# Kernel tuning notes

Hardware: AMD Instinct MI355X
Metric: run time of the kernel (lower is better)

Reference implementation:

```python
import jax, jax.numpy as jnp
import numpy as np

B = 64        # number of tasks (sequential steps)
D = 512       # knowledge_representation_dim == understanding_representation_dim
M = 8192      # memory_slots
GAMMA = 0.95  # memory_gamma


def setup_inputs() -> dict:
    key = jax.random.key(0)
    k1, k2, k3, k4 = jax.random.split(key, 4)
    ortho = jax.nn.initializers.orthogonal()
    return {
        "k": jax.random.normal(k1, (B, 1, D), jnp.float32),
        "u": jax.random.normal(k2, (B, 1, D), jnp.float32),
        "memory_knowledge": ortho(k3, (D, M), jnp.float32),
        "memory_understanding": ortho(k4, (D, M), jnp.float32),
        "beta_param": jnp.float32(0.0),
        "memory_gamma": jnp.float32(GAMMA),
    }


def reference(k, u, memory_knowledge, memory_understanding, beta_param, memory_gamma):
    n_slots = memory_knowledge.shape[1]
    slot_ids = jnp.arange(n_slots)
    beta = jax.nn.sigmoid(beta_param)

    def step(carry, xs):
        MK, MU, w_w, w_u, w_lu = carry
        k_task, u_task = xs  # each [1, D]
        # cosine similarity of the task key against every memory column: [1, M]
        sim = (k_task @ MK) / (
            jnp.linalg.norm(k_task, axis=-1, keepdims=True)
            * jnp.linalg.norm(MK, axis=0, keepdims=True)
        )
        w_r = jax.nn.softmax(sim, axis=-1)[0]  # [M]
        # zero out the least-used slot (argmin of usage weights)
        keep = (slot_ids != jnp.argmin(w_u))[None, :]  # [1, M]
        MK = jnp.where(keep, MK, 0.0)
        MU = jnp.where(keep, MU, 0.0)
        # usage / write / least-used weight updates
        w_u = memory_gamma * w_u + w_r + w_w
        w_w = beta * jnp.mean(w_r) + (1.0 - beta) * w_lu  # [M] via broadcast of scalar mean
        w_lu = (slot_ids == jnp.argmin(w_u)).astype(MK.dtype)  # one-hot least-used
        # rank-1 write of understanding, then read refined understanding, then write knowledge
        MU = MU + u_task[0][:, None] * w_w[None, :]  # [D, M]
        u_ref = w_r @ MK.T  # [D] -- read uses MK after zeroing, before its write
        MK = MK + k_task[0][:, None] * w_w[None, :]  # [D, M]
        return (MK, MU, w_w, w_u, w_lu), u_ref

    zeros = jnp.zeros((n_slots,), memory_knowledge.dtype)
    init = (memory_knowledge, memory_understanding, zeros, zeros, zeros)
    _, u_refined = jax.lax.scan(step, init, (k, u))
    return u_refined[:, None, :]  # [B, 1, D]
```

## Files before the change

### kernel.cpp

```cpp
#include <hip/hip_runtime.h>
#include <math.h>

#define BB 64
#define DD 512
#define MM 8192
#define K2T 512
#define K2C 16

typedef unsigned long long u64;

template<int CTRL>
__device__ __forceinline__ float dpp_addf(float x) {
    int y = __builtin_amdgcn_update_dpp(0, __float_as_int(x), CTRL, 0xF, 0xF, true);
    return x + __int_as_float(y);
}
__device__ __forceinline__ float wave_sum64(float x) {
    x = dpp_addf<0x111>(x); x = dpp_addf<0x112>(x); x = dpp_addf<0x114>(x); x = dpp_addf<0x118>(x);
    x = dpp_addf<0x142>(x); x = dpp_addf<0x143>(x);
    return __int_as_float(__builtin_amdgcn_readlane(__float_as_int(x), 63));
}
template<int CTRL>
__device__ __forceinline__ u64 dpp_min_step(u64 k) {
    unsigned lo = (unsigned)k, hi = (unsigned)(k >> 32);
    unsigned nlo = (unsigned)__builtin_amdgcn_update_dpp((int)0xFFFFFFFFu, (int)lo, CTRL, 0xF, 0xF, false);
    unsigned nhi = (unsigned)__builtin_amdgcn_update_dpp((int)0xFFFFFFFFu, (int)hi, CTRL, 0xF, 0xF, false);
    u64 nk = (((u64)nhi) << 32) | (u64)nlo;
    return nk < k ? nk : k;
}
__device__ __forceinline__ u64 wave_min64_lane63(u64 k) {
    k = dpp_min_step<0x111>(k); k = dpp_min_step<0x112>(k); k = dpp_min_step<0x114>(k);
    k = dpp_min_step<0x118>(k); k = dpp_min_step<0x142>(k); k = dpp_min_step<0x143>(k);
    return k;
}
__device__ __forceinline__ u64 wave_min8(u64 k) {
    k = dpp_min_step<0x111>(k); k = dpp_min_step<0x112>(k); k = dpp_min_step<0x114>(k);
    unsigned lo = (unsigned)__builtin_amdgcn_readlane((int)(unsigned)k, 7);
    unsigned hi = (unsigned)__builtin_amdgcn_readlane((int)(unsigned)(k >> 32), 7);
    return (((u64)hi) << 32) | (u64)lo;
}
__device__ __forceinline__ float readlane_f(float v, int l) {
    return __int_as_float(__builtin_amdgcn_readlane(__float_as_int(v), l));
}

struct K0Smem {
    float Ks[BB][129];
    float Gs[BB][BB];
};
struct K1Smem {
    float Ks[64 * 65];
    float Ms[64 * 65];
    float sq[4 * 64];
};
#define KA_SMEM ((sizeof(K0Smem) > sizeof(K1Smem)) ? sizeof(K0Smem) : sizeof(K1Smem))

__global__ __launch_bounds__(256) void ka_gram_s0(const float* __restrict__ K, const float* __restrict__ MK0,
                                                  float* __restrict__ G, float* __restrict__ Pfx,
                                                  float* __restrict__ S0p, float* __restrict__ n2p) {
    __shared__ __align__(16) char blob[KA_SMEM];
    const int tid = threadIdx.x;

    if (blockIdx.x == 0) {
        K0Smem* sm = (K0Smem*)blob;
        const int ti = ((tid >> 4) & 15) << 2;
        const int tj = (tid & 15) << 2;
        float acc[4][4];
        #pragma unroll
        for (int i = 0; i < 4; ++i)
            #pragma unroll
            for (int j = 0; j < 4; ++j) acc[i][j] = 0.f;
        for (int d0 = 0; d0 < DD; d0 += 128) {
            #pragma unroll
            for (int i = 0; i < 32; ++i) {
                int e = i * 256 + tid; int r = e >> 7, c = e & 127;
                sm->Ks[r][c] = K[r * DD + d0 + c];
            }
            __syncthreads();
            for (int dl = 0; dl < 128; ++dl) {
                float rv[4], cv[4];
                #pragma unroll
                for (int i = 0; i < 4; ++i) rv[i] = sm->Ks[ti + i][dl];
                #pragma unroll
                for (int j = 0; j < 4; ++j) cv[j] = sm->Ks[tj + j][dl];
                #pragma unroll
                for (int i = 0; i < 4; ++i)
                    #pragma unroll
                    for (int j = 0; j < 4; ++j) acc[i][j] += rv[i] * cv[j];
            }
            __syncthreads();
        }
        #pragma unroll
        for (int i = 0; i < 4; ++i)
            #pragma unroll
            for (int j = 0; j < 4; ++j) {
                G[(ti + i) * BB + tj + j] = acc[i][j];
                sm->Gs[ti + i][tj + j] = acc[i][j];
            }
        __syncthreads();
        const int s = tid & 63, w = tid >> 6;
        for (int rr = 0; rr < 16; ++rr) {
            int row = w * 16 + rr;
            float x = (s < row) ? sm->Gs[row][s] : 0.f;
            #pragma unroll
            for (int o = 1; o < 64; o <<= 1) {
                float y = __shfl_down(x, o);
                if (s + o < 64) x += y;
            }
            Pfx[row * BB + s] = x;
        }
        return;
    }

    K1Smem* sm = (K1Smem*)blob;
    const int b = blockIdx.x - 1;
    const int lane = tid & 63, w = tid >> 6;
    const int jb = (b & 127) * 64;
    const int by = b >> 7;
    const int dbase = by * 256;
    const int t4 = ((w << 2) | (lane >> 4)) << 2;
    const int jq0 = lane & 15;
    float acc[4][4];
    #pragma unroll
    for (int i = 0; i < 4; ++i)
        #pragma unroll
        for (int q = 0; q < 4; ++q) acc[i][q] = 0.f;
    float sqa = 0.f;
    for (int dt = 0; dt < 4; ++dt) {
        int d0 = dbase + dt * 64;
        #pragma unroll
        for (int i = 0; i < 16; ++i) {
            int e = i * 256 + tid; int r = e >> 6, c = e & 63;
            sm->Ks[r * 65 + c] = K[r * DD + d0 + c];
            float m = MK0[(d0 + r) * MM + jb + c];
            sm->Ms[r * 65 + c] = m;
            sqa += m * m;
        }
        __syncthreads();
        #pragma unroll 4
        for (int dl = 0; dl < 64; ++dl) {
            float kv[4], mv[4];
            #pragma unroll
            for (int i = 0; i < 4; ++i) kv[i] = sm->Ks[(t4 + i) * 65 + dl];
            #pragma unroll
            for (int q = 0; q < 4; ++q) mv[q] = sm->Ms[dl * 65 + jq0 + 16 * q];
            #pragma unroll
            for (int i = 0; i < 4; ++i)
                #pragma unroll
                for (int q = 0; q < 4; ++q) acc[i][q] += kv[i] * mv[q];
        }
        __syncthreads();
    }
    #pragma unroll
    for (int i = 0; i < 4; ++i)
        #pragma unroll
        for (int q = 0; q < 4; ++q)
            S0p[by * BB * MM + (t4 + i) * MM + jb + jq0 + 16 * q] = acc[i][q];
    sm->sq[w * 64 + lane] = sqa;
    __syncthreads();
    if (w == 0) n2p[by * MM + jb + lane] =
        sm->sq[lane] + sm->sq[64 + lane] + sm->sq[128 + lane] + sm->sq[192 + lane];
}

__global__ __launch_bounds__(256) void k1b_ecold(const float* __restrict__ S0p,
                                                 const float* __restrict__ G,
                                                 const float* __restrict__ Pfx,
                                                 const float* __restrict__ n2p,
                                                 const float* __restrict__ bp,
                                                 float* __restrict__ Ecold) {
    __shared__ float Pfx0s[BB], invks[BB], k2s[BB];
    int tid = threadIdx.x;
    int j = blockIdx.x * 256 + tid;
    if (tid < BB) {
        float g = G[tid * BB + tid];
        k2s[tid] = g;
        invks[tid] = __builtin_amdgcn_rsqf(g);
        Pfx0s[tid] = Pfx[tid * BB + 0];
    }
    const float beta = 1.f / (1.f + expf(-bp[0]));
    const float cuni = beta / (float)MM;
    float n2c = n2p[j] + n2p[MM + j];
    __syncthreads();
    for (int t = 0; t < BB; ++t) {
        float s0 = S0p[t * MM + j] + S0p[(BB + t) * MM + j];
        float d_ = s0 + cuni * Pfx0s[t];
        float cosv = d_ * invks[t] * __builtin_amdgcn_rsqf(n2c);
        float ee = __expf(cosv);
        Ecold[t * MM + j] = ee;
        n2c = n2c + 2.f * cuni * d_ + cuni * cuni * k2s[t];
    }
}

__global__ __launch_bounds__(256) void ks_rowsum(const float* __restrict__ Ecold, float* __restrict__ Scold) {
    __shared__ float sw[4];
    int t = blockIdx.x, tid = threadIdx.x;
    int lane = tid & 63, wid = tid >> 6;
    float s = 0.f;
    #pragma unroll
    for (int i = 0; i < 32; ++i) s += Ecold[t * MM + i * 256 + tid];
    #pragma unroll
    for (int o = 32; o > 0; o >>= 1) s += __shfl_down(s, o);
    if (lane == 0) sw[wid] = s;
    __syncthreads();
    if (tid == 0) Scold[t] = sw[0] + sw[1] + sw[2] + sw[3];
}

struct ScanSmem {
    u64   red[2][8];
    float EtabL[BB * BB];
    float EcTabL[BB * BB];
    float invSL[BB];
    float SL[BB];
    int   endL[BB];
    float invS_bc;
};
struct K3Smem {
    float Ws[64 * 65];
    float Msub[64 * 65];
};
#define SMEM_BYTES ((sizeof(ScanSmem) > sizeof(K3Smem)) ? sizeof(ScanSmem) : sizeof(K3Smem))

__global__ __launch_bounds__(512) void k23_scan_u1(const float* __restrict__ Ecold,
                                                   const float* __restrict__ G,
                                                   const float* __restrict__ Pfx,
                                                   const float* __restrict__ Scoldg,
                                                   const float* __restrict__ bp,
                                                   const float* __restrict__ gp,
                                                   const float* __restrict__ MK0,
                                                   float* __restrict__ Etab_g,
                                                   float* __restrict__ EcTab_g,
                                                   float* __restrict__ Sg,
                                                   float* __restrict__ invSg,
                                                   int*   __restrict__ endTab_g,
                                                   int*   __restrict__ hcolg,
                                                   float* __restrict__ parts) {
    __shared__ __align__(16) char smem_raw[SMEM_BYTES];
    const int tid = threadIdx.x;

    if (blockIdx.x != 0) {
        K3Smem* sm = (K3Smem*)smem_raw;
        const int tile = blockIdx.x - 1;
        const int d0 = (tile & 7) * 64;
        const int by = tile >> 3;
        const bool act = tid < 256;
        const int lane = tid & 63, w = tid >> 6;
        const int t4 = ((w << 2) | (lane >> 4)) << 2;
        const int dq0 = lane & 15;
        float acc[4][4];
        #pragma unroll
        for (int i = 0; i < 4; ++i)
            #pragma unroll
            for (int q = 0; q < 4; ++q) acc[i][q] = 0.f;
        for (int sub = 0; sub < 4; ++sub) {
            int jb = by * 256 + sub * 64;
            if (act) {
                #pragma unroll
                for (int i = 0; i < 16; ++i) {
                    int e = i * 256 + tid; int r = e >> 6, c = e & 63;
                    sm->Ws[r * 65 + c] = Ecold[r * MM + jb + c];
                    sm->Msub[r * 65 + c] = MK0[(d0 + r) * MM + jb + c];
                }
            }
            __syncthreads();
            if (act) {
                #pragma unroll 4
                for (int jl = 0; jl < 64; ++jl) {
                    float wv[4], mv[4];
                    #pragma unroll
                    for (int i = 0; i < 4; ++i) wv[i] = sm->Ws[(t4 + i) * 65 + jl];
                    #pragma unroll
                    for (int q = 0; q < 4; ++q) mv[q] = sm->Msub[(dq0 + 16 * q) * 65 + jl];
                    #pragma unroll
                    for (int i = 0; i < 4; ++i)
                        #pragma unroll
                        for (int q = 0; q < 4; ++q) acc[i][q] += wv[i] * mv[q];
                }
            }
            __syncthreads();
        }
        if (act) {
            #pragma unroll
            for (int i = 0; i < 4; ++i)
                #pragma unroll
                for (int q = 0; q < 4; ++q)
                    parts[(by * 64 + t4 + i) * DD + d0 + dq0 + 16 * q] = acc[i][q];
        }
        return;
    }

    ScanSmem* sm = (ScanSmem*)smem_raw;
    const int lane = tid & 63;
    const int wid = tid >> 6;
    const bool w0 = (wid == 0);

    const float beta  = 1.f / (1.f + expf(-bp[0]));
    const float gamma = gp[0];
    const float cuni  = beta / (float)MM;
    const float omb   = 1.f - beta;

    if (tid < BB) sm->endL[tid] = BB;

    const float4* Ec4 = reinterpret_cast<const float4*>(Ecold);

    float wu[K2C], eb0[K2C], eb1[K2C];
    #pragma unroll
    for (int c = 0; c < K2C; ++c) wu[c] = 0.f;
    #pragma unroll
    for (int i = 0; i < K2C / 4; ++i) {
        float4 v = Ec4[i * K2T + tid];
        eb0[4 * i + 0] = v.x; eb0[4 * i + 1] = v.y; eb0[4 * i + 2] = v.z; eb0[4 * i + 3] = v.w;
    }

    float slot_n2 = 0.f, slot_E = 0.f, slot_ec = 0.f, slot_ecpf = 0.f, wu_hot = 0.f;
    int   slot_j = -1;
    bool  slot_act = false;

    float grow_c = 0.f, pfx_c = 0.f, Ssc_c = 0.f;
    if (w0) { grow_c = G[lane]; pfx_c = Pfx[lane]; Ssc_c = Scoldg[0]; }
    __syncthreads();

    auto step = [&](int t, float (&cur)[K2C], float (&nxt)[K2C]) {
        int j0; float minval;
        if (t == 0) { j0 = 0; minval = 0.f; }
        else {
            u64 pm = sm->red[t & 1][lane & 7];
            pm = wave_min8(pm);
            j0 = (int)(pm & 0xFFFFFFFFu);
            minval = __uint_as_float((unsigned)(pm >> 32));
        }
        const float cuni_t = (t == 0) ? 0.f : cuni;

        float latev = 0.f;
        if (w0 && lane == t) latev = Ecold[t * MM + j0];
        if (w0 && t + 1 < BB) {
            int js = (lane == t) ? j0 : slot_j;
            if (slot_act || lane == t) slot_ecpf = Ecold[(t + 1) * MM + js];
        }
        float grow_n = 0.f, pfx_n = 0.f, Ssc_n = 0.f;
        if (w0 && t + 1 < BB) {
            grow_n = G[(t + 1) * BB + lane];
            pfx_n  = Pfx[(t + 1) * BB + lane];
            Ssc_n  = Scoldg[t + 1];
        }
        __builtin_amdgcn_sched_barrier(0);
        if (t + 1 < BB) {
            #pragma unroll
            for (int i = 0; i < K2C / 4; ++i) {
                float4 v = Ec4[(t + 1) * (MM / 4) + i * K2T + tid];
                nxt[4 * i + 0] = v.x; nxt[4 * i + 1] = v.y; nxt[4 * i + 2] = v.z; nxt[4 * i + 3] = v.w;
            }
        }
        __builtin_amdgcn_sched_barrier(0);

        float invS = 0.f, S = 0.f, e_true = 0.f;
        bool fresh = false;
        if (w0) {
            const float k2t  = readlane_f(grow_c, t);
            const float invk = __builtin_amdgcn_rsqf(k2t);

            u64 sup = __ballot(slot_act && (slot_j == j0));
            const bool has_sup = (sup != 0ull);
            const int  ssup = has_sup ? (int)__builtin_ctzll(sup) : 0;

            float myDelta = 0.f;
            if (slot_act) {
                float d_ = cuni * pfx_c;
                if (lane >= 1) d_ += omb * grow_c;
                e_true = __expf(d_ * invk * __builtin_amdgcn_rsqf(slot_n2));
                myDelta = e_true - slot_ec;
                slot_E = e_true;
                slot_n2 = slot_n2 + 2.f * cuni * d_ + cuni * cuni * k2t;
            }

            S = Ssc_c + wave_sum64(myDelta);
            invS = __builtin_amdgcn_rcpf(S);
            sm->invS_bc = invS;

            if (slot_act) {
                float ww = cuni + ((t >= 2 && lane == t - 1) ? omb : 0.f);
                wu_hot = fmaf(gamma, wu_hot, fmaf(e_true, invS, ww));
            }

            float trans_wu = readlane_f(wu_hot, ssup);
            float trans_E  = readlane_f(e_true, ssup);
            if (lane == t) {
                slot_j = j0;
                float ww0 = cuni + ((t >= 1) ? omb : 0.f);
                slot_n2 = ww0 * ww0 * k2t;
                slot_act = true;
                if (has_sup) { wu_hot = trans_wu; slot_E = trans_E; }
                fresh = !has_sup;
            }
            if (has_sup) {
                if (lane == ssup) slot_act = false;
                if (lane == t) sm->endL[ssup] = t;
            }
        }

        asm volatile("s_waitcnt lgkmcnt(0)" ::: "memory");
        __builtin_amdgcn_s_barrier();
        asm volatile("" ::: "memory");
        if (!w0) invS = sm->invS_bc;

        float vmin = 0.f; int jmin = 0;
        #pragma unroll
        for (int i = 0; i < 4; ++i) {
            #pragma unroll
            for (int q = 0; q < 4; ++q) {
                int c = i * 4 + q;
                float wun = fmaf(gamma, wu[c], fmaf(cur[c], invS, cuni_t));
                wu[c] = wun;
                int j = i * 2048 + (tid << 2) + q;
                if (c == 0) { vmin = wun; jmin = j; }
                else if (wun < vmin) { vmin = wun; jmin = j; }
            }
        }
        u64 key = (((u64)__float_as_uint(vmin)) << 32) | (unsigned)jmin;

        if (((j0 >> 2) & (K2T - 1)) == tid) {
            int cj = ((j0 >> 11) << 2) | (j0 & 3);
            #pragma unroll
            for (int c = 0; c < K2C; ++c) if (c == cj) wu[c] = __builtin_inff();
        }

        if (w0) {
            u64 skey = (slot_act && !fresh)
                     ? ((((u64)__float_as_uint(wu_hot)) << 32) | (unsigned)slot_j) : ~0ull;
            key = skey < key ? skey : key;
        }
        key = wave_min64_lane63(key);
        if (lane == 63) sm->red[(t + 1) & 1][wid] = key;

        if (w0) {
            if (lane == t) slot_ec = latev;
            if (fresh) {
                slot_E  = latev;
                wu_hot  = fmaf(gamma, minval, fmaf(latev, invS, cuni_t));
            }
            sm->EtabL[t * BB + lane]  = slot_E;
            sm->EcTabL[t * BB + lane] = slot_ec;
            if (lane == 0) { sm->invSL[t] = invS; sm->SL[t] = S; }
            if (slot_act) slot_ec = slot_ecpf;
            grow_c = grow_n; pfx_c = pfx_n; Ssc_c = Ssc_n;
        }

        asm volatile("s_waitcnt lgkmcnt(0)" ::: "memory");
        __builtin_amdgcn_s_barrier();
        asm volatile("" ::: "memory");
    };

    #pragma unroll 1
    for (int th = 0; th < BB; th += 2) {
        step(th, eb0, eb1);
        step(th + 1, eb1, eb0);
    }

    for (int i = tid; i < BB * BB; i += K2T) {
        Etab_g[i]  = sm->EtabL[i];
        EcTab_g[i] = sm->EcTabL[i];
    }
    if (tid < BB) {
        Sg[tid] = sm->SL[tid];
        invSg[tid] = sm->invSL[tid];
        endTab_g[tid] = sm->endL[tid];
    }
    if (w0) hcolg[lane] = slot_j;
}

__global__ __launch_bounds__(512) void k3b_gather(const float* __restrict__ MK0, const int* __restrict__ hcolg,
                                                  float* __restrict__ MKhot) {
    int i = blockIdx.x, d = threadIdx.x;
    int h = hcolg[i];
    MKhot[i * DD + d] = MK0[d * MM + h];
}

__global__ __launch_bounds__(512) void k4_final(const float* __restrict__ parts,
                                                const float* __restrict__ K,
                                                const float* __restrict__ Etab,
                                                const float* __restrict__ EcTab,
                                                const int*   __restrict__ endTab,
                                                const float* __restrict__ Sg,
                                                const float* __restrict__ invSg,
                                                const float* __restrict__ MKhot,
                                                const float* __restrict__ bp,
                                                float* __restrict__ out) {
    __shared__ float Arow[BB];
    __shared__ float Drow[BB];
    int t = blockIdx.x, d = threadIdx.x;
    if (d < BB) {
        const float beta = 1.f / (1.f + expf(-bp[0]));
        const float cuni = beta / (float)MM;
        const float omb  = 1.f - beta;
        int s = d;
        float Ev = Etab[t * BB + s];
        int endv = endTab[s];
        bool act = (s <= t) && (t < endv);
        float S = Sg[t], invS = invSg[t];
        float ev = act ? Ev : 0.f;
        float x = ev;
        #pragma unroll
        for (int o = 1; o < 64; o <<= 1) {
            float y = __shfl_down(x, o);
            if (s + o < 64) x += y;
        }
        float suf = x - ev;
        float arow = 0.f;
        if (s < t) {
            float Qe = S - suf;
            arow = cuni * Qe;
            if (s >= 1 && act) arow += omb * Ev;
            arow *= invS;
        }
        Arow[s] = arow;
        Drow[s] = act ? (-invS * EcTab[t * BB + s]) : 0.f;
    }
    __syncthreads();
    float isv = invSg[t];
    float s1 = 0.f;
    #pragma unroll
    for (int p = 0; p < 32; ++p) s1 += parts[(p * 64 + t) * DD + d];
    float s2 = 0.f;
    for (int i = 0; i < BB; ++i) s2 += Drow[i] * MKhot[i * DD + d];
    float s3 = 0.f;
    for (int i = 0; i < BB; ++i) s3 += Arow[i] * K[i * DD + d];
    out[t * DD + d] = isv * s1 + s2 + s3;
}

extern "C" void kernel_launch(void* const* d_in, const int* in_sizes, int n_in,
                              void* d_out, int out_size, void* d_ws, size_t ws_size,
                              hipStream_t stream) {
    const float* K   = (const float*)d_in[0];
    const float* MK0 = (const float*)d_in[2];
    const float* bp  = (const float*)d_in[4];
    const float* gp  = (const float*)d_in[5];

    float* ws    = (float*)d_ws;
    float* G     = ws;
    float* Pfx   = G + 4096;
    float* S0p   = Pfx + 4096;
    float* n2p   = S0p + 1048576;
    float* Ecold = n2p + 16384;
    float* Scold = Ecold + 524288;
    float* Etab  = Scold + 64;
    float* EcTab = Etab + 4096;
    float* Sarr  = EcTab + 4096;
    float* invS  = Sarr + 64;
    float* MKhot = invS + 64;
    float* parts = MKhot + 32768;
    int*   hcol  = (int*)(parts + 1048576);
    int*   endT  = hcol + 64;
    float* out   = (float*)d_out;

    ka_gram_s0  <<<257, 256, 0, stream>>>(K, MK0, G, Pfx, S0p, n2p);
    k1b_ecold   <<<32, 256, 0, stream>>>(S0p, G, Pfx, n2p, bp, Ecold);
    ks_rowsum   <<<64, 256, 0, stream>>>(Ecold, Scold);
    k23_scan_u1 <<<257, 512, 0, stream>>>(Ecold, G, Pfx, Scold, bp, gp, MK0,
                                          Etab, EcTab, Sarr, invS, endT, hcol, parts);
    k3b_gather  <<<64, 512, 0, stream>>>(MK0, hcol, MKhot);
    k4_final    <<<64, 512, 0, stream>>>(parts, K, Etab, EcTab, endT, Sarr, invS, MKhot, bp, out);
}
```

Before: 220.8 us.

## Deepen scan prefetch, tree-reduce argmin, widen ecold grid, store tables directly

The scan block now prefetches Ecold rows two steps ahead using a three-buffer rotation, and replaces the sequential per-thread argmin with a pairwise tree over packed 64-bit keys. Per-step tables go straight to global memory instead of being staged in shared memory and copied out at the end. k1b_ecold runs 128 blocks of 64 threads with software-prefetched S0p loads, and the GEMM side of k23 drops to 255 worker blocks that loop over tiles. The aim is to shorten the serial scan's critical path and spread the ecold pass over more CUs, at the cost of extra registers and uneven GEMM tile distribution.

```diff
diff --git a/kernel.cpp b/kernel.cpp
--- a/kernel.cpp
+++ b/kernel.cpp
@@ -160,16 +160,16 @@
         sm->sq[lane] + sm->sq[64 + lane] + sm->sq[128 + lane] + sm->sq[192 + lane];
 }
 
-__global__ __launch_bounds__(256) void k1b_ecold(const float* __restrict__ S0p,
-                                                 const float* __restrict__ G,
-                                                 const float* __restrict__ Pfx,
-                                                 const float* __restrict__ n2p,
-                                                 const float* __restrict__ bp,
-                                                 float* __restrict__ Ecold) {
+__global__ __launch_bounds__(64) void k1b_ecold(const float* __restrict__ S0p,
+                                                const float* __restrict__ G,
+                                                const float* __restrict__ Pfx,
+                                                const float* __restrict__ n2p,
+                                                const float* __restrict__ bp,
+                                                float* __restrict__ Ecold) {
     __shared__ float Pfx0s[BB], invks[BB], k2s[BB];
     int tid = threadIdx.x;
-    int j = blockIdx.x * 256 + tid;
-    if (tid < BB) {
+    int j = blockIdx.x * 64 + tid;
+    {
         float g = G[tid * BB + tid];
         k2s[tid] = g;
         invks[tid] = __builtin_amdgcn_rsqf(g);
@@ -179,13 +179,21 @@
     const float cuni = beta / (float)MM;
     float n2c = n2p[j] + n2p[MM + j];
     __syncthreads();
+    float pa = S0p[j];
+    float pb = S0p[BB * MM + j];
     for (int t = 0; t < BB; ++t) {
-        float s0 = S0p[t * MM + j] + S0p[(BB + t) * MM + j];
+        float na = 0.f, nb = 0.f;
+        if (t + 1 < BB) {
+            na = S0p[(t + 1) * MM + j];
+            nb = S0p[(BB + t + 1) * MM + j];
+        }
+        float s0 = pa + pb;
         float d_ = s0 + cuni * Pfx0s[t];
         float cosv = d_ * invks[t] * __builtin_amdgcn_rsqf(n2c);
         float ee = __expf(cosv);
         Ecold[t * MM + j] = ee;
         n2c = n2c + 2.f * cuni * d_ + cuni * cuni * k2s[t];
+        pa = na; pb = nb;
     }
 }
 
@@ -205,10 +213,6 @@
 
 struct ScanSmem {
     u64   red[2][8];
-    float EtabL[BB * BB];
-    float EcTabL[BB * BB];
-    float invSL[BB];
-    float SL[BB];
     int   endL[BB];
     float invS_bc;
 };
@@ -237,51 +241,53 @@
 
     if (blockIdx.x != 0) {
         K3Smem* sm = (K3Smem*)smem_raw;
-        const int tile = blockIdx.x - 1;
-        const int d0 = (tile & 7) * 64;
-        const int by = tile >> 3;
-        const bool act = tid < 256;
-        const int lane = tid & 63, w = tid >> 6;
-        const int t4 = ((w << 2) | (lane >> 4)) << 2;
-        const int dq0 = lane & 15;
-        float acc[4][4];
-        #pragma unroll
-        for (int i = 0; i < 4; ++i)
-            #pragma unroll
-            for (int q = 0; q < 4; ++q) acc[i][q] = 0.f;
-        for (int sub = 0; sub < 4; ++sub) {
-            int jb = by * 256 + sub * 64;
+        for (int tile = blockIdx.x - 1; tile < 256; tile += 255) {
+            const int d0 = (tile & 7) * 64;
+            const int by = tile >> 3;
+            const bool act = tid < 256;
+            const int lane = tid & 63, w = tid >> 6;
+            const int t4 = ((w << 2) | (lane >> 4)) << 2;
+            const int dq0 = lane & 15;
+            float acc[4][4];
+            #pragma unroll
+            for (int i = 0; i < 4; ++i)
+                #pragma unroll
+                for (int q = 0; q < 4; ++q) acc[i][q] = 0.f;
+            for (int sub = 0; sub < 4; ++sub) {
+                int jb = by * 256 + sub * 64;
+                if (act) {
+                    #pragma unroll
+                    for (int i = 0; i < 16; ++i) {
+                        int e = i * 256 + tid; int r = e >> 6, c = e & 63;
+                        sm->Ws[r * 65 + c] = Ecold[r * MM + jb + c];
+                        sm->Msub[r * 65 + c] = MK0[(d0 + r) * MM + jb + c];
+                    }
+                }
+                __syncthreads();
+                if (act) {
+                    #pragma unroll 4
+                    for (int jl = 0; jl < 64; ++jl) {
+                        float wv[4], mv[4];
+                        #pragma unroll
+                        for (int i = 0; i < 4; ++i) wv[i] = sm->Ws[(t4 + i) * 65 + jl];
+                        #pragma unroll
+                        for (int q = 0; q < 4; ++q) mv[q] = sm->Msub[(dq0 + 16 * q) * 65 + jl];
+                        #pragma unroll
+                        for (int i = 0; i < 4; ++i)
+                            #pragma unroll
+                            for (int q = 0; q < 4; ++q) acc[i][q] += wv[i] * mv[q];
+                    }
+                }
+                __syncthreads();
+            }
             if (act) {
                 #pragma unroll
-                for (int i = 0; i < 16; ++i) {
-                    int e = i * 256 + tid; int r = e >> 6, c = e & 63;
-                    sm->Ws[r * 65 + c] = Ecold[r * MM + jb + c];
-                    sm->Msub[r * 65 + c] = MK0[(d0 + r) * MM + jb + c];
-                }
+                for (int i = 0; i < 4; ++i)
+                    #pragma unroll
+                    for (int q = 0; q < 4; ++q)
+                        parts[(by * 64 + t4 + i) * DD + d0 + dq0 + 16 * q] = acc[i][q];
             }
             __syncthreads();
-            if (act) {
-                #pragma unroll 4
-                for (int jl = 0; jl < 64; ++jl) {
-                    float wv[4], mv[4];
-                    #pragma unroll
-                    for (int i = 0; i < 4; ++i) wv[i] = sm->Ws[(t4 + i) * 65 + jl];
-                    #pragma unroll
-                    for (int q = 0; q < 4; ++q) mv[q] = sm->Msub[(dq0 + 16 * q) * 65 + jl];
-                    #pragma unroll
-                    for (int i = 0; i < 4; ++i)
-                        #pragma unroll
-                        for (int q = 0; q < 4; ++q) acc[i][q] += wv[i] * mv[q];
-                }
-            }
-            __syncthreads();
-        }
-        if (act) {
-            #pragma unroll
-            for (int i = 0; i < 4; ++i)
-                #pragma unroll
-                for (int q = 0; q < 4; ++q)
-                    parts[(by * 64 + t4 + i) * DD + d0 + dq0 + 16 * q] = acc[i][q];
         }
         return;
     }
@@ -300,13 +306,15 @@
 
     const float4* Ec4 = reinterpret_cast<const float4*>(Ecold);
 
-    float wu[K2C], eb0[K2C], eb1[K2C];
+    float wu[K2C], e0[K2C], e1[K2C], e2[K2C];
     #pragma unroll
     for (int c = 0; c < K2C; ++c) wu[c] = 0.f;
     #pragma unroll
     for (int i = 0; i < K2C / 4; ++i) {
         float4 v = Ec4[i * K2T + tid];
-        eb0[4 * i + 0] = v.x; eb0[4 * i + 1] = v.y; eb0[4 * i + 2] = v.z; eb0[4 * i + 3] = v.w;
+        e0[4 * i + 0] = v.x; e0[4 * i + 1] = v.y; e0[4 * i + 2] = v.z; e0[4 * i + 3] = v.w;
+        float4 u = Ec4[(MM / 4) + i * K2T + tid];
+        e1[4 * i + 0] = u.x; e1[4 * i + 1] = u.y; e1[4 * i + 2] = u.z; e1[4 * i + 3] = u.w;
     }
 
     float slot_n2 = 0.f, slot_E = 0.f, slot_ec = 0.f, slot_ecpf = 0.f, wu_hot = 0.f;
@@ -317,7 +325,7 @@
     if (w0) { grow_c = G[lane]; pfx_c = Pfx[lane]; Ssc_c = Scoldg[0]; }
     __syncthreads();
 
-    auto step = [&](int t, float (&cur)[K2C], float (&nxt)[K2C]) {
+    auto step = [&](int t, float (&cur)[K2C], float (&ld)[K2C]) {
         int j0; float minval;
         if (t == 0) { j0 = 0; minval = 0.f; }
         else {
@@ -341,11 +349,11 @@
             Ssc_n  = Scoldg[t + 1];
         }
         __builtin_amdgcn_sched_barrier(0);
-        if (t + 1 < BB) {
+        if (t + 2 < BB) {
             #pragma unroll
             for (int i = 0; i < K2C / 4; ++i) {
-                float4 v = Ec4[(t + 1) * (MM / 4) + i * K2T + tid];
-                nxt[4 * i + 0] = v.x; nxt[4 * i + 1] = v.y; nxt[4 * i + 2] = v.z; nxt[4 * i + 3] = v.w;
+                float4 v = Ec4[(t + 2) * (MM / 4) + i * K2T + tid];
+                ld[4 * i + 0] = v.x; ld[4 * i + 1] = v.y; ld[4 * i + 2] = v.z; ld[4 * i + 3] = v.w;
             }
         }
         __builtin_amdgcn_sched_barrier(0);
@@ -400,7 +408,7 @@
         asm volatile("" ::: "memory");
         if (!w0) invS = sm->invS_bc;
 
-        float vmin = 0.f; int jmin = 0;
+        u64 kk[K2C];
         #pragma unroll
         for (int i = 0; i < 4; ++i) {
             #pragma unroll
@@ -409,11 +417,15 @@
                 float wun = fmaf(gamma, wu[c], fmaf(cur[c], invS, cuni_t));
                 wu[c] = wun;
                 int j = i * 2048 + (tid << 2) + q;
-                if (c == 0) { vmin = wun; jmin = j; }
-                else if (wun < vmin) { vmin = wun; jmin = j; }
-            }
-        }
-        u64 key = (((u64)__float_as_uint(vmin)) << 32) | (unsigned)jmin;
+                kk[c] = (((u64)__float_as_uint(wun)) << 32) | (unsigned)j;
+            }
+        }
+        #pragma unroll
+        for (int s = 8; s >= 1; s >>= 1)
+            #pragma unroll
+            for (int c = 0; c < s; ++c)
+                kk[c] = kk[c + s] < kk[c] ? kk[c + s] : kk[c];
+        u64 key = kk[0];
 
         if (((j0 >> 2) & (K2T - 1)) == tid) {
             int cj = ((j0 >> 11) << 2) | (j0 & 3);
@@ -435,9 +447,9 @@
                 slot_E  = latev;
                 wu_hot  = fmaf(gamma, minval, fmaf(latev, invS, cuni_t));
             }
-            sm->EtabL[t * BB + lane]  = slot_E;
-            sm->EcTabL[t * BB + lane] = slot_ec;
-            if (lane == 0) { sm->invSL[t] = invS; sm->SL[t] = S; }
+            Etab_g[t * BB + lane]  = slot_E;
+            EcTab_g[t * BB + lane] = slot_ec;
+            if (lane == 0) { invSg[t] = invS; Sg[t] = S; }
             if (slot_act) slot_ec = slot_ecpf;
             grow_c = grow_n; pfx_c = pfx_n; Ssc_c = Ssc_n;
         }
@@ -448,20 +460,14 @@
     };
 
     #pragma unroll 1
-    for (int th = 0; th < BB; th += 2) {
-        step(th, eb0, eb1);
-        step(th + 1, eb1, eb0);
-    }
-
-    for (int i = tid; i < BB * BB; i += K2T) {
-        Etab_g[i]  = sm->EtabL[i];
-        EcTab_g[i] = sm->EcTabL[i];
-    }
-    if (tid < BB) {
-        Sg[tid] = sm->SL[tid];
-        invSg[tid] = sm->invSL[tid];
-        endTab_g[tid] = sm->endL[tid];
-    }
+    for (int th = 0; th < 63; th += 3) {
+        step(th + 0, e0, e2);
+        step(th + 1, e1, e0);
+        step(th + 2, e2, e1);
+    }
+    step(63, e0, e2);
+
+    if (tid < BB) endTab_g[tid] = sm->endL[tid];
     if (w0) hcolg[lane] = slot_j;
 }
 
@@ -550,9 +556,9 @@
     float* out   = (float*)d_out;
 
     ka_gram_s0  <<<257, 256, 0, stream>>>(K, MK0, G, Pfx, S0p, n2p);
-    k1b_ecold   <<<32, 256, 0, stream>>>(S0p, G, Pfx, n2p, bp, Ecold);
+    k1b_ecold   <<<128, 64, 0, stream>>>(S0p, G, Pfx, n2p, bp, Ecold);
     ks_rowsum   <<<64, 256, 0, stream>>>(Ecold, Scold);
-    k23_scan_u1 <<<257, 512, 0, stream>>>(Ecold, G, Pfx, Scold, bp, gp, MK0,
+    k23_scan_u1 <<<256, 512, 0, stream>>>(Ecold, G, Pfx, Scold, bp, gp, MK0,
                                           Etab, EcTab, Sarr, invS, endT, hcol, parts);
     k3b_gather  <<<64, 512, 0, stream>>>(MK0, hcol, MKhot);
     k4_final    <<<64, 512, 0, stream>>>(parts, K, Etab, EcTab, endT, Sarr, invS, MKhot, bp, out);
```

Measured after the change: 225.1 us. About the same (+1.9%).
